# Kernel optimization log

Measured on AMD Instinct MI355X. Metric: run time of the kernel, lower is better.

## Reference

```python
import jax, jax.numpy as jnp
import numpy as np
from jax import lax

B, T, K = 2048, 1024, 8  # batch, max seq len, num_tags


def setup_inputs() -> dict:
    key = jax.random.key(0)
    k1, k2, k3, k4, k5, k6, k7 = jax.random.split(key, 7)
    score = jax.random.normal(k1, (B, T, K), jnp.float32)
    log_p = jax.nn.log_softmax(jax.random.normal(k2, (B, T, K), jnp.float32), axis=-1)
    tags = jax.random.randint(k3, (B, T), 0, K)
    seq_l = jax.random.randint(k4, (B,), 1, T + 1)  # valid lengths in [1, T]
    transitions = jax.random.normal(k5, (K, K), jnp.float32) * 0.1
    start_transitions = jax.random.normal(k6, (K,), jnp.float32) * 0.1
    end_transitions = jax.random.normal(k7, (K,), jnp.float32) * 0.1
    return {
        "log_p": log_p,
        "score": score,
        "transitions": transitions,
        "start_transitions": start_transitions,
        "end_transitions": end_transitions,
        "tags": tags,
        "seq_l": seq_l,
    }


def _crf_nll(score, tags, mask, transitions, start_transitions, end_transitions):
    """Linear-chain CRF negative log-likelihood, summed over the batch.
    score: [B,T,K] emissions; tags: [B,T] gold; mask: [B,T] bool."""
    maskf = mask.astype(score.dtype)

    # ---- numerator: score of the gold tag path ----
    emit = jnp.take_along_axis(score, tags[..., None], axis=-1)[..., 0]  # [B,T]
    num = (emit * maskf).sum(-1)
    num = num + start_transitions[tags[:, 0]]
    trans_sc = transitions[tags[:, :-1], tags[:, 1:]]  # [B,T-1]
    num = num + (trans_sc * maskf[:, 1:]).sum(-1)
    last_idx = (mask.sum(-1).astype(jnp.int32) - 1)  # [B]
    last_tag = jnp.take_along_axis(tags, last_idx[:, None], axis=1)[:, 0]
    num = num + end_transitions[last_tag]

    # ---- denominator: log partition via log-sum-exp scan over time ----
    alpha0 = start_transitions[None, :] + score[:, 0]  # [B,K]

    def step(alpha, xs):
        emit_t, mask_t = xs  # [B,K], [B]
        # alpha[b,i] + transitions[i,j] + emit[b,j], logsumexp over i
        nxt = jax.nn.logsumexp(alpha[:, :, None] + transitions[None, :, :], axis=1) + emit_t
        alpha = jnp.where(mask_t[:, None], nxt, alpha)  # freeze past end-of-seq
        return alpha, None

    xs = (jnp.swapaxes(score[:, 1:], 0, 1), jnp.swapaxes(mask[:, 1:], 0, 1))
    alpha, _ = lax.scan(step, alpha0, xs)
    log_z = jax.nn.logsumexp(alpha + end_transitions[None, :], axis=-1)  # [B]

    return -(num - log_z).sum()


def reference(log_p, score, transitions, start_transitions, end_transitions, tags, seq_l):
    mask = jnp.arange(T)[None, :] < seq_l[:, None]  # [B,T] bool
    loss = _crf_nll(score, tags, mask, transitions, start_transitions, end_transitions) / B
    # training path: quick predictions = argmax over per-token log_p, zero-padded
    pred_idx = jnp.argmax(log_p, axis=-1) * mask.astype(jnp.int64)
    return loss, pred_idx
```

## Files before the change

### kernel.cpp

```cpp
#include <hip/hip_runtime.h>
#include <hip/hip_bf16.h>


namespace {

constexpr int B = 2048;
constexpr int T = 1024;
constexpr int NC = 64;

__device__ __forceinline__ float max8(const float* a) {
  return fmaxf(fmaxf(fmaxf(a[0], a[1]), fmaxf(a[2], a[3])),
               fmaxf(fmaxf(a[4], a[5]), fmaxf(a[6], a[7])));
}

__global__ void init_kernel(const float* __restrict__ trans,
                            float* __restrict__ expE,
                            float* __restrict__ ws_num,
                            float* __restrict__ out0) {
  int i = threadIdx.x;
  for (int r = i; r < B; r += 256) ws_num[r] = 0.0f;
  if (i < 64) expE[i] = __expf(trans[i]);
  if (i == 64) *out0 = 0.0f;
}

__global__ __launch_bounds__(256) void pred_num_kernel(
    const float* __restrict__ log_p, const float* __restrict__ score,
    const float* __restrict__ trans, const float* __restrict__ start_tr,
    const float* __restrict__ end_tr, const int* __restrict__ tags,
    const int* __restrict__ seq_l, float* __restrict__ out_pred,
    float* __restrict__ ws_num) {
  int tid = blockIdx.x * blockDim.x + threadIdx.x;
  int g0 = tid << 2;
  int b = g0 >> 10;
  int t0 = g0 & (T - 1);
  int L = seq_l[b];

  const float4* lp = reinterpret_cast<const float4*>(log_p) + (g0 << 1);
  float4 u[8];
#pragma unroll
  for (int r = 0; r < 8; ++r) u[r] = lp[r];
  int4 tg4 = *reinterpret_cast<const int4*>(tags + g0);
  int tg[4] = {tg4.x, tg4.y, tg4.z, tg4.w};
  int prev0 = (t0 == 0) ? 0 : tags[g0 - 1];

  float contrib = 0.0f;
#pragma unroll
  for (int r = 0; r < 4; ++r) {
    float v[8] = {u[2 * r].x, u[2 * r].y, u[2 * r].z, u[2 * r].w,
                  u[2 * r + 1].x, u[2 * r + 1].y, u[2 * r + 1].z,
                  u[2 * r + 1].w};
    int best = 0;
    float bv = v[0];
#pragma unroll
    for (int j = 1; j < 8; ++j) {
      if (v[j] > bv) { bv = v[j]; best = j; }
    }
    int t = t0 + r;
    bool act = (t < L);
    out_pred[g0 + r] = act ? (float)best : 0.0f;
    if (act) {
      int tgr = tg[r];
      float csum = score[(size_t)(g0 + r) * 8 + tgr];
      if (t == 0)
        csum += start_tr[tgr];
      else
        csum += trans[((r == 0) ? prev0 : tg[r - 1]) * 8 + tgr];
      if (t == L - 1) csum += end_tr[tgr];
      contrib += csum;
    }
  }
#pragma unroll
  for (int off = 32; off >= 1; off >>= 1) contrib += __shfl_down(contrib, off);
  if ((threadIdx.x & 63) == 0) atomicAdd(&ws_num[b], contrib);
}

__global__ __launch_bounds__(64) void chunk_kernel(
    const float* __restrict__ score, const float* __restrict__ expE,
    const int* __restrict__ seq_l, float* __restrict__ wsA,
    float* __restrict__ wsS) {
  float E[64];
#pragma unroll
  for (int i = 0; i < 64; ++i) E[i] = expE[i];

  int wid = blockIdx.x;
  int braw = wid >> 3;
  int oct = wid & 7;
  int b = (int)(((unsigned)braw * 1229u) & 2047u);

  int lane = threadIdx.x & 63;
  int grp = lane >> 3;
  int k = lane & 7;
  int c = oct * 8 + grp;

  int S = seq_l[b] - 1;
  int ts = 1 + ((S * c) >> 6);
  int te = 1 + ((S * (c + 1)) >> 6);
  int n = te - ts;

  float a[8];
#pragma unroll
  for (int j = 0; j < 8; ++j) a[j] = (j == k) ? 1.0f : 0.0f;
  float sig = 0.0f;

  const float* sp = score + ((size_t)b * T + ts) * 8;
  float4 nA, nB;
  if (n > 0) {
    nA = *reinterpret_cast<const float4*>(sp);
    nB = *reinterpret_cast<const float4*>(sp + 4);
  }
  for (int it = 0; it < n; ++it) {
    float4 cA = nA, cB = nB;
    if (it + 1 < n) {
      nA = *reinterpret_cast<const float4*>(sp + 8);
      nB = *reinterpret_cast<const float4*>(sp + 12);
    }
    sp += 8;
    float em[8] = {__expf(cA.x), __expf(cA.y), __expf(cA.z), __expf(cA.w),
                   __expf(cB.x), __expf(cB.y), __expf(cB.z), __expf(cB.w)};
    float na[8];
#pragma unroll
    for (int j = 0; j < 8; ++j) {
      float acc = E[0 * 8 + j] * a[0];
#pragma unroll
      for (int i = 1; i < 8; ++i) acc = fmaf(E[i * 8 + j], a[i], acc);
      na[j] = em[j] * acc;
    }
#pragma unroll
    for (int j = 0; j < 8; ++j) a[j] = na[j];
    if ((it & 7) == 7) {
      float mm = max8(a);
      float r = __builtin_amdgcn_rcpf(mm);
#pragma unroll
      for (int j = 0; j < 8; ++j) a[j] *= r;
      sig += __logf(mm);
    }
  }
  {
    float mm = max8(a);
    if (mm > 0.0f) {
      float r = __builtin_amdgcn_rcpf(mm);
#pragma unroll
      for (int j = 0; j < 8; ++j) a[j] *= r;
      sig += __logf(mm);
    }
  }

  float* Ao = wsA + (size_t)(b * NC + c) * 64;
#pragma unroll
  for (int j = 0; j < 8; ++j) Ao[j * 8 + k] = a[j];
  wsS[(b * NC + c) * 8 + k] = sig;
}

__global__ __launch_bounds__(256) void combine_kernel(
    const float* __restrict__ score, const float* __restrict__ start_tr,
    const float* __restrict__ end_tr, const float* __restrict__ wsA,
    const float* __restrict__ wsS, const float* __restrict__ ws_num,
    float* __restrict__ out_loss) {
  __shared__ float sm[96 * 73];
  int b = blockIdx.x;
  int tid = threadIdx.x;
  const float* Ab = wsA + (size_t)b * NC * 64;
  const float* Sb = wsS + (size_t)b * NC * 8;

#pragma unroll
  for (int r = 0; r < 4; ++r) {
    int vi = tid + r * 256;
    int g = vi * 4;
    int c = g >> 6, rem = g & 63;
    float4 q = reinterpret_cast<const float4*>(Ab)[vi];
    float* dst = &sm[c * 73 + rem];
    dst[0] = q.x; dst[1] = q.y; dst[2] = q.z; dst[3] = q.w;
  }
#pragma unroll
  for (int r = 0; r < 2; ++r) {
    int gi = tid + r * 256;
    sm[(gi >> 3) * 73 + 64 + (gi & 7)] = Sb[gi];
  }
  __syncthreads();

  float* bufB = &sm[64 * 73];
  int p = tid >> 3, k = tid & 7;
#pragma unroll
  for (int lvl = 1; lvl <= 6; ++lvl) {
    int nprod = NC >> lvl;
    float* inb = (lvl & 1) ? sm : bufB;
    float* outb = (lvl & 1) ? bufB : sm;
    if (p < nprod) {
      const float* M0 = inb + (size_t)(2 * p) * 73;
      const float* M1 = inb + (size_t)(2 * p + 1) * 73;
      float s1[8];
#pragma unroll
      for (int i = 0; i < 8; ++i) s1[i] = M1[64 + i];
      float m = max8(s1);
      float w[8];
#pragma unroll
      for (int i = 0; i < 8; ++i) w[i] = M0[i * 8 + k] * __expf(s1[i] - m);
      float u[8];
#pragma unroll
      for (int j = 0; j < 8; ++j) {
        float acc = M1[j * 8 + 0] * w[0];
#pragma unroll
        for (int i = 1; i < 8; ++i) acc = fmaf(M1[j * 8 + i], w[i], acc);
        u[j] = acc;
      }
      float mm = fmaxf(max8(u), 1e-37f);
      float rc = __builtin_amdgcn_rcpf(mm);
      float* D = outb + (size_t)p * 73;
#pragma unroll
      for (int j = 0; j < 8; ++j) D[j * 8 + k] = u[j] * rc;
      D[64 + k] = M0[64 + k] + m + __logf(mm);
    }
    __syncthreads();
  }

  if (tid < 8) {
    int j = tid;
    float p0 = __expf(start_tr[j] + score[(size_t)b * T * 8 + j]);
    float m0 = p0;
#pragma unroll
    for (int m = 1; m < 8; m <<= 1) m0 = fmaxf(m0, __shfl_xor(m0, m, 8));
    float p0n = p0 * __builtin_amdgcn_rcpf(m0);
    float p0a[8];
#pragma unroll
    for (int i = 0; i < 8; ++i) p0a[i] = __shfl(p0n, i, 8);
    float sM[8];
#pragma unroll
    for (int i = 0; i < 8; ++i) sM[i] = sm[64 + i];
    float mS = max8(sM);
    float inner = 0.0f;
#pragma unroll
    for (int i = 0; i < 8; ++i)
      inner = fmaf(sm[j * 8 + i], __expf(sM[i] - mS) * p0a[i], inner);
    float term = inner * __expf(end_tr[j]);
#pragma unroll
    for (int m = 1; m < 8; m <<= 1) term += __shfl_xor(term, m, 8);
    if (j == 0) {
      float logz = __logf(m0) + mS + __logf(term);
      atomicAdd(out_loss, (logz - ws_num[b]) * (1.0f / (float)B));
    }
  }
}

}

extern "C" void kernel_launch(void* const* d_in, const int* in_sizes, int n_in,
                              void* d_out, int out_size, void* d_ws,
                              size_t ws_size, hipStream_t stream) {
  const float* log_p = (const float*)d_in[0];
  const float* score = (const float*)d_in[1];
  const float* trans = (const float*)d_in[2];
  const float* start_tr = (const float*)d_in[3];
  const float* end_tr = (const float*)d_in[4];
  const int* tags = (const int*)d_in[5];
  const int* seq_l = (const int*)d_in[6];
  float* out = (float*)d_out;

  float* wsA = (float*)d_ws;
  float* wsS = wsA + (size_t)B * NC * 64;
  float* wsNum = wsS + (size_t)B * NC * 8;
  float* wsExpE = wsNum + B;

  init_kernel<<<1, 256, 0, stream>>>(trans, wsExpE, wsNum, out);
  pred_num_kernel<<<(B * T / 4) / 256, 256, 0, stream>>>(
      log_p, score, trans, start_tr, end_tr, tags, seq_l, out + 1, wsNum);
  chunk_kernel<<<B * NC / 8, 64, 0, stream>>>(score, wsExpE, seq_l, wsA, wsS);
  combine_kernel<<<B, 256, 0, stream>>>(score, start_tr, end_tr, wsA, wsS,
                                        wsNum, out);
}
```

Measured before the change: 231.2 us.

## Fuse gold-path numerator into chunk scan and merge pred/chunk kernels

The separate init, prediction/numerator and chunk kernels are merged into one launch. The gold-path score is computed by the lane-0 thread of each chunk group while it streams the same score rows, so score is no longer read a second time. The remaining blocks only do the argmax prediction. exp(transitions) is computed per block instead of in an init kernel, and the zeroing is done with memsets. The cost is serialized tag and transition loads on one lane per group inside the recurrence loop, which could lengthen the latency-bound chunk scan.

```diff
diff --git a/kernel.cpp b/kernel.cpp
--- a/kernel.cpp
+++ b/kernel.cpp
@@ -7,148 +7,188 @@
 constexpr int B = 2048;
 constexpr int T = 1024;
 constexpr int NC = 64;
+constexpr int CHUNK_BLOCKS = B * 2;
+constexpr int PRED_BLOCKS = (B * T / 4) / 256;
 
 __device__ __forceinline__ float max8(const float* a) {
   return fmaxf(fmaxf(fmaxf(a[0], a[1]), fmaxf(a[2], a[3])),
                fmaxf(fmaxf(a[4], a[5]), fmaxf(a[6], a[7])));
 }
 
-__global__ void init_kernel(const float* __restrict__ trans,
-                            float* __restrict__ expE,
-                            float* __restrict__ ws_num,
-                            float* __restrict__ out0) {
-  int i = threadIdx.x;
-  for (int r = i; r < B; r += 256) ws_num[r] = 0.0f;
-  if (i < 64) expE[i] = __expf(trans[i]);
-  if (i == 64) *out0 = 0.0f;
-}
-
-__global__ __launch_bounds__(256) void pred_num_kernel(
+__device__ __forceinline__ float uniform_f(float v) {
+  return __int_as_float(__builtin_amdgcn_readfirstlane(__float_as_int(v)));
+}
+
+__device__ __forceinline__ float sel8(float4 A, float4 B, int idx) {
+  float lo = (idx & 1) ? ((idx & 2) ? A.w : A.y) : ((idx & 2) ? A.z : A.x);
+  float hi = (idx & 1) ? ((idx & 2) ? B.w : B.y) : ((idx & 2) ? B.z : B.x);
+  return (idx & 4) ? hi : lo;
+}
+
+__global__ __launch_bounds__(256) void fused_kernel(
     const float* __restrict__ log_p, const float* __restrict__ score,
     const float* __restrict__ trans, const float* __restrict__ start_tr,
     const float* __restrict__ end_tr, const int* __restrict__ tags,
     const int* __restrict__ seq_l, float* __restrict__ out_pred,
-    float* __restrict__ ws_num) {
-  int tid = blockIdx.x * blockDim.x + threadIdx.x;
-  int g0 = tid << 2;
-  int b = g0 >> 10;
-  int t0 = g0 & (T - 1);
-  int L = seq_l[b];
-
-  const float4* lp = reinterpret_cast<const float4*>(log_p) + (g0 << 1);
-  float4 u[8];
-#pragma unroll
-  for (int r = 0; r < 8; ++r) u[r] = lp[r];
-  int4 tg4 = *reinterpret_cast<const int4*>(tags + g0);
-  int tg[4] = {tg4.x, tg4.y, tg4.z, tg4.w};
-  int prev0 = (t0 == 0) ? 0 : tags[g0 - 1];
-
-  float contrib = 0.0f;
-#pragma unroll
-  for (int r = 0; r < 4; ++r) {
-    float v[8] = {u[2 * r].x, u[2 * r].y, u[2 * r].z, u[2 * r].w,
-                  u[2 * r + 1].x, u[2 * r + 1].y, u[2 * r + 1].z,
-                  u[2 * r + 1].w};
-    int best = 0;
-    float bv = v[0];
-#pragma unroll
-    for (int j = 1; j < 8; ++j) {
-      if (v[j] > bv) { bv = v[j]; best = j; }
-    }
-    int t = t0 + r;
-    bool act = (t < L);
-    out_pred[g0 + r] = act ? (float)best : 0.0f;
-    if (act) {
-      int tgr = tg[r];
-      float csum = score[(size_t)(g0 + r) * 8 + tgr];
-      if (t == 0)
-        csum += start_tr[tgr];
-      else
-        csum += trans[((r == 0) ? prev0 : tg[r - 1]) * 8 + tgr];
-      if (t == L - 1) csum += end_tr[tgr];
-      contrib += csum;
-    }
-  }
-#pragma unroll
-  for (int off = 32; off >= 1; off >>= 1) contrib += __shfl_down(contrib, off);
-  if ((threadIdx.x & 63) == 0) atomicAdd(&ws_num[b], contrib);
-}
-
-__global__ __launch_bounds__(64) void chunk_kernel(
-    const float* __restrict__ score, const float* __restrict__ expE,
-    const int* __restrict__ seq_l, float* __restrict__ wsA,
+    float* __restrict__ ws_num, float* __restrict__ wsA,
     float* __restrict__ wsS) {
-  float E[64];
-#pragma unroll
-  for (int i = 0; i < 64; ++i) E[i] = expE[i];
-
-  int wid = blockIdx.x;
-  int braw = wid >> 3;
-  int oct = wid & 7;
-  int b = (int)(((unsigned)braw * 1229u) & 2047u);
-
-  int lane = threadIdx.x & 63;
-  int grp = lane >> 3;
-  int k = lane & 7;
-  int c = oct * 8 + grp;
-
-  int S = seq_l[b] - 1;
-  int ts = 1 + ((S * c) >> 6);
-  int te = 1 + ((S * (c + 1)) >> 6);
-  int n = te - ts;
-
-  float a[8];
-#pragma unroll
-  for (int j = 0; j < 8; ++j) a[j] = (j == k) ? 1.0f : 0.0f;
-  float sig = 0.0f;
-
-  const float* sp = score + ((size_t)b * T + ts) * 8;
-  float4 nA, nB;
-  if (n > 0) {
-    nA = *reinterpret_cast<const float4*>(sp);
-    nB = *reinterpret_cast<const float4*>(sp + 4);
-  }
-  for (int it = 0; it < n; ++it) {
-    float4 cA = nA, cB = nB;
-    if (it + 1 < n) {
-      nA = *reinterpret_cast<const float4*>(sp + 8);
-      nB = *reinterpret_cast<const float4*>(sp + 12);
-    }
-    sp += 8;
-    float em[8] = {__expf(cA.x), __expf(cA.y), __expf(cA.z), __expf(cA.w),
-                   __expf(cB.x), __expf(cB.y), __expf(cB.z), __expf(cB.w)};
-    float na[8];
-#pragma unroll
-    for (int j = 0; j < 8; ++j) {
-      float acc = E[0 * 8 + j] * a[0];
-#pragma unroll
-      for (int i = 1; i < 8; ++i) acc = fmaf(E[i * 8 + j], a[i], acc);
-      na[j] = em[j] * acc;
-    }
-#pragma unroll
-    for (int j = 0; j < 8; ++j) a[j] = na[j];
-    if ((it & 7) == 7) {
+  int bid = blockIdx.x;
+  if (bid < CHUNK_BLOCKS) {
+    int braw = bid >> 1;
+    int half = bid & 1;
+    int b = (int)(((unsigned)braw * 1229u) & 2047u);
+    int wave = threadIdx.x >> 6;
+    int lane = threadIdx.x & 63;
+    int grp = lane >> 3;
+    int k = lane & 7;
+    int c = (half * 4 + wave) * 8 + grp;
+
+    float E[64];
+#pragma unroll
+    for (int i = 0; i < 64; ++i) E[i] = uniform_f(__expf(trans[i]));
+
+    int L = seq_l[b];
+    int S = L - 1;
+    int ts = 1 + ((S * c) >> 6);
+    int te = 1 + ((S * (c + 1)) >> 6);
+    int n = te - ts;
+
+    float a[8];
+#pragma unroll
+    for (int j = 0; j < 8; ++j) a[j] = (j == k) ? 1.0f : 0.0f;
+    float sig = 0.0f;
+
+    const float* sp = score + ((size_t)b * T + ts) * 8;
+    const int* tprow = tags + (size_t)b * T;
+
+    float num = 0.0f;
+    int prev = 0, tc0 = 0, tc1 = 0, tc2 = 0, tc3 = 0;
+    if (k == 0) {
+      if (c == 0) {
+        int tg0 = tprow[0];
+        num += score[(size_t)b * T * 8 + tg0] + start_tr[tg0];
+      }
+      if (n > 0) {
+        prev = tprow[ts - 1];
+        tc0 = tprow[min(ts + 0, T - 1)];
+        tc1 = tprow[min(ts + 1, T - 1)];
+        tc2 = tprow[min(ts + 2, T - 1)];
+        tc3 = tprow[min(ts + 3, T - 1)];
+      }
+    }
+
+    int nblk = (n + 3) >> 2;
+    float4 nA, nB;
+    if (n > 0) {
+      nA = *reinterpret_cast<const float4*>(sp);
+      nB = *reinterpret_cast<const float4*>(sp + 4);
+    }
+    int t = ts;
+    int done = 0;
+    for (int blk = 0; blk < nblk; ++blk) {
+      int rem = n - done;
+      int nt0 = 0, nt1 = 0, nt2 = 0, nt3 = 0;
+      float tr0 = 0.0f, tr1 = 0.0f, tr2 = 0.0f, tr3 = 0.0f;
+      if (k == 0) {
+        if (blk + 1 < nblk) {
+          nt0 = tprow[min(t + 4, T - 1)];
+          nt1 = tprow[min(t + 5, T - 1)];
+          nt2 = tprow[min(t + 6, T - 1)];
+          nt3 = tprow[min(t + 7, T - 1)];
+        }
+        tr0 = trans[prev * 8 + tc0];
+        if (rem > 1) tr1 = trans[tc0 * 8 + tc1];
+        if (rem > 2) tr2 = trans[tc1 * 8 + tc2];
+        if (rem > 3) tr3 = trans[tc2 * 8 + tc3];
+      }
+#pragma unroll
+      for (int s = 0; s < 4; ++s) {
+        if (s >= rem) break;
+        float4 cA = nA, cB = nB;
+        if (done + s + 1 < n) {
+          nA = *reinterpret_cast<const float4*>(sp + 8);
+          nB = *reinterpret_cast<const float4*>(sp + 12);
+        }
+        sp += 8;
+        if (k == 0) {
+          int tgs = (s == 0) ? tc0 : (s == 1) ? tc1 : (s == 2) ? tc2 : tc3;
+          num += sel8(cA, cB, tgs);
+        }
+        float em[8] = {__expf(cA.x), __expf(cA.y), __expf(cA.z), __expf(cA.w),
+                       __expf(cB.x), __expf(cB.y), __expf(cB.z), __expf(cB.w)};
+        float na[8];
+#pragma unroll
+        for (int j = 0; j < 8; ++j) {
+          float acc = E[0 * 8 + j] * a[0];
+#pragma unroll
+          for (int i = 1; i < 8; ++i) acc = fmaf(E[i * 8 + j], a[i], acc);
+          na[j] = em[j] * acc;
+        }
+#pragma unroll
+        for (int j = 0; j < 8; ++j) a[j] = na[j];
+      }
+      if (k == 0) {
+        num += tr0 + tr1 + tr2 + tr3;
+        prev = (rem > 3) ? tc3 : (rem == 3) ? tc2 : (rem == 2) ? tc1 : tc0;
+        tc0 = nt0; tc1 = nt1; tc2 = nt2; tc3 = nt3;
+      }
+      if (blk & 1) {
+        float mm = max8(a);
+        float r = __builtin_amdgcn_rcpf(mm);
+#pragma unroll
+        for (int j = 0; j < 8; ++j) a[j] *= r;
+        sig += __logf(mm);
+      }
+      done += 4;
+      t += 4;
+    }
+    {
       float mm = max8(a);
-      float r = __builtin_amdgcn_rcpf(mm);
-#pragma unroll
-      for (int j = 0; j < 8; ++j) a[j] *= r;
-      sig += __logf(mm);
-    }
-  }
-  {
-    float mm = max8(a);
-    if (mm > 0.0f) {
-      float r = __builtin_amdgcn_rcpf(mm);
-#pragma unroll
-      for (int j = 0; j < 8; ++j) a[j] *= r;
-      sig += __logf(mm);
-    }
-  }
-
-  float* Ao = wsA + (size_t)(b * NC + c) * 64;
-#pragma unroll
-  for (int j = 0; j < 8; ++j) Ao[j * 8 + k] = a[j];
-  wsS[(b * NC + c) * 8 + k] = sig;
+      if (mm > 0.0f) {
+        float r = __builtin_amdgcn_rcpf(mm);
+#pragma unroll
+        for (int j = 0; j < 8; ++j) a[j] *= r;
+        sig += __logf(mm);
+      }
+    }
+    if (k == 0 && c == NC - 1) {
+      num += end_tr[tprow[te - 1]];
+    }
+
+    float* Ao = wsA + (size_t)(b * NC + c) * 64;
+#pragma unroll
+    for (int j = 0; j < 8; ++j) Ao[j * 8 + k] = a[j];
+    wsS[(b * NC + c) * 8 + k] = sig;
+
+    float part = (k == 0) ? num : 0.0f;
+#pragma unroll
+    for (int off = 32; off >= 1; off >>= 1) part += __shfl_down(part, off);
+    if (lane == 0) atomicAdd(&ws_num[b], part);
+  } else {
+    int tid = (bid - CHUNK_BLOCKS) * 256 + threadIdx.x;
+    int g0 = tid << 2;
+    int b = g0 >> 10;
+    int t0 = g0 & (T - 1);
+    int L = seq_l[b];
+
+    const float4* lp = reinterpret_cast<const float4*>(log_p) + (g0 << 1);
+    float4 u[8];
+#pragma unroll
+    for (int r = 0; r < 8; ++r) u[r] = lp[r];
+#pragma unroll
+    for (int r = 0; r < 4; ++r) {
+      float v[8] = {u[2 * r].x, u[2 * r].y, u[2 * r].z, u[2 * r].w,
+                    u[2 * r + 1].x, u[2 * r + 1].y, u[2 * r + 1].z,
+                    u[2 * r + 1].w};
+      int best = 0;
+      float bv = v[0];
+#pragma unroll
+      for (int j = 1; j < 8; ++j) {
+        if (v[j] > bv) { bv = v[j]; best = j; }
+      }
+      out_pred[g0 + r] = (t0 + r < L) ? (float)best : 0.0f;
+    }
+  }
 }
 
 __global__ __launch_bounds__(256) void combine_kernel(
@@ -258,12 +298,13 @@
   float* wsA = (float*)d_ws;
   float* wsS = wsA + (size_t)B * NC * 64;
   float* wsNum = wsS + (size_t)B * NC * 8;
-  float* wsExpE = wsNum + B;
-
-  init_kernel<<<1, 256, 0, stream>>>(trans, wsExpE, wsNum, out);
-  pred_num_kernel<<<(B * T / 4) / 256, 256, 0, stream>>>(
-      log_p, score, trans, start_tr, end_tr, tags, seq_l, out + 1, wsNum);
-  chunk_kernel<<<B * NC / 8, 64, 0, stream>>>(score, wsExpE, seq_l, wsA, wsS);
+
+  hipMemsetAsync(wsNum, 0, B * sizeof(float), stream);
+  hipMemsetAsync(out, 0, sizeof(float), stream);
+
+  fused_kernel<<<CHUNK_BLOCKS + PRED_BLOCKS, 256, 0, stream>>>(
+      log_p, score, trans, start_tr, end_tr, tags, seq_l, out + 1, wsNum,
+      wsA, wsS);
   combine_kernel<<<B, 256, 0, stream>>>(score, start_tr, end_tr, wsA, wsS,
                                         wsNum, out);
 }
```

After: 233.2 us. No clear change (+0.9%).
